# Optimization experiments

Hardware: AMD Instinct MI355X
Metric: run time of the kernel (lower is better)

Reference implementation:

```python
import jax, jax.numpy as jnp
import numpy as np

HID, HEADS, FF, DEPTH = 1152, 16, 4304, 2
HD = HID // HEADS            # 72
ROT = HD // 2                # 36 (rotary_pos_emb width)
S, NSEG = 2048, 4
EPS = 1e-6


def _layernorm(x, w, b):
    m = jnp.mean(x, axis=-1, keepdims=True)
    xc = x - m
    v = jnp.mean(xc * xc, axis=-1, keepdims=True)
    return xc * jax.lax.rsqrt(v + EPS) * w + b


def _rotate_half(x):
    x1, x2 = jnp.split(x, 2, axis=-1)
    return jnp.concatenate([-x2, x1], axis=-1)


def _apply_rotary(t, freqs):
    # t: [S, H, D], freqs: [S, D/2]
    emb = jnp.concatenate([freqs, freqs], axis=-1)          # [S, D]
    cos = jnp.cos(emb)[:, None, :]
    sin = jnp.sin(emb)[:, None, :]
    return t * cos + _rotate_half(t) * sin


def setup_inputs() -> dict:
    key = jax.random.key(0)
    ks = jax.random.split(key, 16)
    sd = 0.02
    # rotary freqs as in VisionRotaryEmbedding(dim=HD//2): h-pos and w-pos halves
    inv_freq = 1.0 / (10000.0 ** (jnp.arange(0, ROT, 2, dtype=jnp.float32) / ROT))  # [18]
    pos = jnp.arange(S, dtype=jnp.float32)
    hpos, wpos = pos // 32.0, pos % 32.0
    rotary = jnp.concatenate([jnp.outer(hpos, inv_freq), jnp.outer(wpos, inv_freq)], axis=-1)  # [S, 36]
    return {
        "x": jax.random.normal(ks[0], (S, HID), jnp.float32),
        "cu_seqlens": jnp.arange(NSEG + 1, dtype=jnp.int32) * (S // NSEG),
        "rotary_pos_emb": rotary,
        "norm1_w": jnp.ones((DEPTH, HID), jnp.float32),
        "norm1_b": jnp.zeros((DEPTH, HID), jnp.float32),
        "qkv_w": jax.random.normal(ks[1], (DEPTH, 3 * HID, HID), jnp.float32) * sd,
        "qkv_b": jnp.zeros((DEPTH, 3 * HID), jnp.float32),
        "proj_w": jax.random.normal(ks[2], (DEPTH, HID, HID), jnp.float32) * sd,
        "proj_b": jnp.zeros((DEPTH, HID), jnp.float32),
        "norm2_w": jnp.ones((DEPTH, HID), jnp.float32),
        "norm2_b": jnp.zeros((DEPTH, HID), jnp.float32),
        "fc1_w": jax.random.normal(ks[3], (DEPTH, FF, HID), jnp.float32) * sd,
        "fc1_b": jnp.zeros((DEPTH, FF), jnp.float32),
        "fc2_w": jax.random.normal(ks[4], (DEPTH, HID, FF), jnp.float32) * sd,
        "fc2_b": jnp.zeros((DEPTH, HID), jnp.float32),
    }


def _forward(x, cu_seqlens, rotary_pos_emb, norm1_w, norm1_b, qkv_w, qkv_b,
             proj_w, proj_b, norm2_w, norm2_b, fc1_w, fc1_b, fc2_w, fc2_b):
    seq_len = x.shape[0]
    # block-diagonal additive mask from cu_seqlens (same mask the torch loop builds)
    seg = jnp.searchsorted(cu_seqlens, jnp.arange(seq_len, dtype=cu_seqlens.dtype), side="right") - 1
    same = seg[:, None] == seg[None, :]
    bias = jnp.where(same, jnp.float32(0.0), jnp.finfo(jnp.float32).min)  # [S, S]
    scale = 1.0 / np.sqrt(HD)
    for d in range(DEPTH):
        # --- attention ---
        h = _layernorm(x, norm1_w[d], norm1_b[d])
        qkv = (h @ qkv_w[d].T + qkv_b[d]).reshape(seq_len, 3, HEADS, HD)
        q, k, v = qkv[:, 0], qkv[:, 1], qkv[:, 2]           # [S, H, D]
        q = _apply_rotary(q, rotary_pos_emb)
        k = _apply_rotary(k, rotary_pos_emb)
        scores = jnp.einsum("qhd,khd->hqk", q, k) * scale + bias[None]
        probs = jax.nn.softmax(scores.astype(jnp.float32), axis=-1).astype(q.dtype)
        attn = jnp.einsum("hqk,khd->qhd", probs, v).reshape(seq_len, HID)
        x = x + attn @ proj_w[d].T + proj_b[d]
        # --- MLP (gelu tanh approx) ---
        h2 = _layernorm(x, norm2_w[d], norm2_b[d])
        x = x + jax.nn.gelu(h2 @ fc1_w[d].T + fc1_b[d], approximate=True) @ fc2_w[d].T + fc2_b[d]
    return x


def reference(x, cu_seqlens, rotary_pos_emb, norm1_w, norm1_b, qkv_w, qkv_b,
              proj_w, proj_b, norm2_w, norm2_b, fc1_w, fc1_b, fc2_w, fc2_b):
    return _forward(x, cu_seqlens, rotary_pos_emb, norm1_w, norm1_b, qkv_w, qkv_b,
                    proj_w, proj_b, norm2_w, norm2_b, fc1_w, fc1_b, fc2_w, fc2_b)
```

## Files before the change

kernel.cpp:

```cpp
#include <hip/hip_runtime.h>

#define S_LEN 2048
#define HID   1152
#define HEADS 16
#define HD    72
#define ROT   36
#define LD3   3456
#define FF    4304
#define FFP   4320

typedef short s16x8 __attribute__((ext_vector_type(8)));
typedef short s16x4 __attribute__((ext_vector_type(4)));
typedef float f32x4 __attribute__((ext_vector_type(4)));
typedef short bf_t;

__device__ __forceinline__ short f2b(float f) {
  unsigned u = __float_as_uint(f);
  u += 0x7fffu + ((u >> 16) & 1u);
  return (short)(u >> 16);
}
__device__ __forceinline__ float b2f(short h) {
  return __uint_as_float(((unsigned)(unsigned short)h) << 16);
}
__device__ __forceinline__ float gelu_f(float x) {
  float t = tanhf(0.7978845608028654f * (x + 0.044715f * x * x * x));
  return 0.5f * x * (1.0f + t);
}

typedef const __attribute__((address_space(1))) void* gas_p;
typedef __attribute__((address_space(3))) void* las_p;
__device__ __forceinline__ void gload16(const void* g, void* l) {
  __builtin_amdgcn_global_load_lds((gas_p)g, (las_p)l, 16, 0, 0);
}

__global__ __launch_bounds__(256) void convw4_kernel(
    const float* __restrict__ src, int N, int K,
    bf_t* __restrict__ dst, int Kpad)
{
  int idx = blockIdx.x * 256 + threadIdx.x;
  int kq = Kpad >> 2;
  if (idx >= N * kq) return;
  int n = idx / kq, k = (idx % kq) << 2;
  s16x4 o;
  if (k + 3 < K) {
    float4 v = *(const float4*)(src + (size_t)n * K + k);
    o[0] = f2b(v.x); o[1] = f2b(v.y); o[2] = f2b(v.z); o[3] = f2b(v.w);
  } else {
#pragma unroll
    for (int j = 0; j < 4; j++) {
      int kk = k + j;
      o[j] = (kk < K) ? f2b(src[(size_t)n * K + kk]) : (short)0;
    }
  }
  *(s16x4*)(dst + (size_t)n * Kpad + k) = o;
}

__global__ __launch_bounds__(256) void costab_kernel(
    const float* __restrict__ rot, float* __restrict__ ct, float* __restrict__ st)
{
  int i = blockIdx.x * 256 + threadIdx.x;
  if (i < S_LEN * ROT) { float f = rot[i]; ct[i] = cosf(f); st[i] = sinf(f); }
}

__global__ __launch_bounds__(256) void ln_kernel(
    const float* __restrict__ x, const float* __restrict__ wgt,
    const float* __restrict__ bia, bf_t* __restrict__ outb)
{
  const int row = blockIdx.x, tid = threadIdx.x;
  const float4* xr = (const float4*)(x + (size_t)row * HID);
  float4 a = xr[tid];
  float4 b2 = make_float4(0.f, 0.f, 0.f, 0.f);
  const bool has2 = tid < 32;
  if (has2) b2 = xr[256 + tid];
  float s = a.x + a.y + a.z + a.w + b2.x + b2.y + b2.z + b2.w;
  float q = a.x*a.x + a.y*a.y + a.z*a.z + a.w*a.w
          + b2.x*b2.x + b2.y*b2.y + b2.z*b2.z + b2.w*b2.w;
  for (int mk = 32; mk; mk >>= 1) { s += __shfl_xor(s, mk); q += __shfl_xor(q, mk); }
  __shared__ float red[16];
  if ((tid & 63) == 0) { red[tid >> 6] = s; red[8 + (tid >> 6)] = q; }
  __syncthreads();
  if (tid == 0) {
    red[4]  = red[0] + red[1] + red[2] + red[3];
    red[12] = red[8] + red[9] + red[10] + red[11];
  }
  __syncthreads();
  float mean = red[4] * (1.0f / HID);
  float var  = red[12] * (1.0f / HID) - mean * mean;
  float rstd = rsqrtf(var + 1e-6f);
  const float4* w4 = (const float4*)wgt;
  const float4* b4 = (const float4*)bia;
  s16x4* o4 = (s16x4*)(outb + (size_t)row * HID);
  {
    float4 wv = w4[tid], bv = b4[tid];
    s16x4 o;
    o[0] = f2b((a.x - mean) * rstd * wv.x + bv.x);
    o[1] = f2b((a.y - mean) * rstd * wv.y + bv.y);
    o[2] = f2b((a.z - mean) * rstd * wv.z + bv.z);
    o[3] = f2b((a.w - mean) * rstd * wv.w + bv.w);
    o4[tid] = o;
  }
  if (has2) {
    float4 wv = w4[256 + tid], bv = b4[256 + tid];
    s16x4 o;
    o[0] = f2b((b2.x - mean) * rstd * wv.x + bv.x);
    o[1] = f2b((b2.y - mean) * rstd * wv.y + bv.y);
    o[2] = f2b((b2.z - mean) * rstd * wv.z + bv.z);
    o[3] = f2b((b2.w - mean) * rstd * wv.w + bv.w);
    o4[256 + tid] = o;
  }
}

__global__ __launch_bounds__(256) void rotary_kernel(
    bf_t* __restrict__ qkv, const float* __restrict__ ct, const float* __restrict__ st)
{
  int idx = blockIdx.x * 256 + threadIdx.x;
  if (idx >= S_LEN * HEADS * ROT) return;
  int t = idx / (HEADS * ROT);
  int r = idx % (HEADS * ROT);
  int h = r / ROT, dd = r % ROT;
  float c = ct[t * ROT + dd], s = st[t * ROT + dd];
  size_t base = (size_t)t * LD3 + h * HD + dd;
  float q1 = b2f(qkv[base]),        q2 = b2f(qkv[base + ROT]);
  float k1 = b2f(qkv[base + HID]),  k2 = b2f(qkv[base + HID + ROT]);
  const float scale = 0.11785113019775793f;
  qkv[base]             = f2b((q1 * c - q2 * s) * scale);
  qkv[base + ROT]       = f2b((q2 * c + q1 * s) * scale);
  qkv[base + HID]       = f2b(k1 * c - k2 * s);
  qkv[base + HID + ROT] = f2b(k2 * c + k1 * s);
}

template<int MODE>
__global__ __launch_bounds__(256, 4) void gemm1(
    const bf_t* __restrict__ A, int lda,
    const bf_t* __restrict__ B, int ldb,
    const float* __restrict__ bias, int nbias,
    void* outp, int ldc, int nvalid, int K, int kchunk)
{
  __shared__ __align__(16) bf_t As[128 * 32];
  __shared__ __align__(16) bf_t Bs[128 * 32];
  const int tid = threadIdx.x;
  const int l = tid & 63, w = tid >> 6;
  const int lr = l & 15, lg = l >> 4;
  const int wm = (w >> 1) * 64, wn = (w & 1) * 64;

  unsigned gx = gridDim.x, gy = gridDim.y, gz = gridDim.z;
  unsigned nwg = gx * gy * gz;
  unsigned lin = (blockIdx.z * gy + blockIdx.y) * gx + blockIdx.x;
  if ((nwg & 7u) == 0u) {
    unsigned q = nwg >> 3;
    lin = (lin & 7u) * q + (lin >> 3);
  }
  const unsigned bz = lin / (gx * gy);
  const unsigned rem = lin % (gx * gy);
  const unsigned by = rem / gx, bx = rem % gx;

  const int rowA0 = by * 128, colB0 = bx * 128;
  const int kb0 = bz * kchunk;
  int kb1 = kb0 + kchunk; if (kb1 > K) kb1 = K;

  const int o1 = tid * 16, o2 = o1 + 4096;
  const int r1 = o1 >> 6, c1 = o1 & 63;
  const int r2 = o2 >> 6, c2 = o2 & 63;
  const char* Ab = (const char*)A;
  const char* Bb = (const char*)B;

  f32x4 acc[4][4] = {};

  for (int kb = kb0; kb < kb1; kb += 32) {
    gload16(Ab + ((size_t)(rowA0 + r1) * lda + kb) * 2 + c1, (char*)As + o1);
    gload16(Ab + ((size_t)(rowA0 + r2) * lda + kb) * 2 + c2, (char*)As + o2);
    gload16(Bb + ((size_t)(colB0 + r1) * ldb + kb) * 2 + c1, (char*)Bs + o1);
    gload16(Bb + ((size_t)(colB0 + r2) * ldb + kb) * 2 + c2, (char*)Bs + o2);
    asm volatile("s_waitcnt vmcnt(0)" ::: "memory");
    __syncthreads();
    s16x8 af[4], bv[4];
#pragma unroll
    for (int mt = 0; mt < 4; mt++) af[mt] = *(const s16x8*)&As[(wm + mt * 16 + lr) * 32 + lg * 8];
#pragma unroll
    for (int nt = 0; nt < 4; nt++) bv[nt] = *(const s16x8*)&Bs[(wn + nt * 16 + lr) * 32 + lg * 8];
#pragma unroll
    for (int mt = 0; mt < 4; mt++)
#pragma unroll
      for (int nt = 0; nt < 4; nt++)
        acc[mt][nt] = __builtin_amdgcn_mfma_f32_16x16x32_bf16(af[mt], bv[nt], acc[mt][nt], 0, 0, 0);
    __syncthreads();
  }

#pragma unroll
  for (int mt = 0; mt < 4; mt++) {
    const int rr = rowA0 + wm + mt * 16 + lg * 4;
#pragma unroll
    for (int nt = 0; nt < 4; nt++) {
      const int cc = colB0 + wn + nt * 16 + lr;
      const float bvl = (MODE == 3) ? 0.0f : ((cc < nbias) ? bias[cc] : 0.0f);
#pragma unroll
      for (int i = 0; i < 4; i++) {
        float v = acc[mt][nt][i] + bvl;
        const int row = rr + i;
        if (MODE == 0) {
          ((bf_t*)outp)[(size_t)row * ldc + cc] = f2b(v);
        } else if (MODE == 2) {
          if (cc < nvalid)      ((bf_t*)outp)[(size_t)row * ldc + cc] = f2b(gelu_f(v));
          else if (cc < ldc)    ((bf_t*)outp)[(size_t)row * ldc + cc] = 0;
        } else {
          float* P = (float*)outp + (size_t)bz * ((size_t)S_LEN * ldc);
          P[(size_t)row * ldc + cc] = v;
        }
      }
    }
  }
}

template<int MODE>
__global__ __launch_bounds__(256, 4) void gemm2(
    const bf_t* __restrict__ A, int lda,
    const bf_t* __restrict__ B, int ldb,
    const float* __restrict__ bias, int nbias,
    void* outp, int ldc, int nvalid, int K, int kchunk)
{
  __shared__ __align__(16) bf_t As[2][128 * 32];
  __shared__ __align__(16) bf_t Bs[2][64 * 32];
  const int tid = threadIdx.x;
  const int l = tid & 63, w = tid >> 6;
  const int lr = l & 15, lg = l >> 4;
  const int wm = (w >> 1) * 64, wn = (w & 1) * 32;

  unsigned gx = gridDim.x, gy = gridDim.y, gz = gridDim.z;
  unsigned nwg = gx * gy * gz;
  unsigned lin = (blockIdx.z * gy + blockIdx.y) * gx + blockIdx.x;
  if ((nwg & 7u) == 0u) {
    unsigned q = nwg >> 3;
    lin = (lin & 7u) * q + (lin >> 3);
  }
  const unsigned bz = lin / (gx * gy);
  const unsigned rem = lin % (gx * gy);
  const unsigned by = rem / gx, bx = rem % gx;

  const int rowA0 = by * 128, colB0 = bx * 64;
  const int kb0 = bz * kchunk;
  int kb1 = kb0 + kchunk; if (kb1 > K) kb1 = K;

  const int oA1 = tid * 16, oA2 = oA1 + 4096;
  const int rA1 = oA1 >> 6, cA1 = oA1 & 63;
  const int rA2 = rA1 + 64;
  const int oB = tid * 16;
  const int rB = oB >> 6, cB = oB & 63;
  const char* Ab = (const char*)A;
  const char* Bb = (const char*)B;

#define STAGE(buf, kk) do { \
    gload16(Ab + ((size_t)(rowA0 + rA1) * lda + (kk)) * 2 + cA1, (char*)As[buf] + oA1); \
    gload16(Ab + ((size_t)(rowA0 + rA2) * lda + (kk)) * 2 + cA1, (char*)As[buf] + oA2); \
    gload16(Bb + ((size_t)(colB0 + rB)  * ldb + (kk)) * 2 + cB,  (char*)Bs[buf] + oB);  \
  } while (0)

  f32x4 acc[4][2] = {};

  STAGE(0, kb0);
  asm volatile("s_waitcnt vmcnt(0)" ::: "memory");
  __builtin_amdgcn_s_barrier();
  __builtin_amdgcn_sched_barrier(0);

  int cur = 0;
  for (int kb = kb0; kb < kb1; kb += 32) {
    if (kb + 32 < kb1) STAGE(cur ^ 1, kb + 32);
    s16x8 af[4], bv[2];
#pragma unroll
    for (int mt = 0; mt < 4; mt++)
      af[mt] = *(const s16x8*)&As[cur][(wm + mt * 16 + lr) * 32 + lg * 8];
#pragma unroll
    for (int nt = 0; nt < 2; nt++)
      bv[nt] = *(const s16x8*)&Bs[cur][(wn + nt * 16 + lr) * 32 + lg * 8];
    asm volatile("s_waitcnt lgkmcnt(0)" ::: "memory");
    __builtin_amdgcn_sched_barrier(0);
#pragma unroll
    for (int mt = 0; mt < 4; mt++)
#pragma unroll
      for (int nt = 0; nt < 2; nt++)
        acc[mt][nt] = __builtin_amdgcn_mfma_f32_16x16x32_bf16(af[mt], bv[nt], acc[mt][nt], 0, 0, 0);
    asm volatile("s_waitcnt vmcnt(0)" ::: "memory");
    __builtin_amdgcn_s_barrier();
    __builtin_amdgcn_sched_barrier(0);
    cur ^= 1;
  }
#undef STAGE

#pragma unroll
  for (int mt = 0; mt < 4; mt++) {
    const int rr = rowA0 + wm + mt * 16 + lg * 4;
#pragma unroll
    for (int nt = 0; nt < 2; nt++) {
      const int cc = colB0 + wn + nt * 16 + lr;
      const float bvl = (cc < nbias) ? bias[cc] : 0.0f;
#pragma unroll
      for (int i = 0; i < 4; i++) {
        float v = acc[mt][nt][i] + bvl;
        const int row = rr + i;
        if (MODE == 0) {
          ((bf_t*)outp)[(size_t)row * ldc + cc] = f2b(v);
        } else if (MODE == 2) {
          if (cc < nvalid)      ((bf_t*)outp)[(size_t)row * ldc + cc] = f2b(gelu_f(v));
          else if (cc < ldc)    ((bf_t*)outp)[(size_t)row * ldc + cc] = 0;
        } else {
          float* P = (float*)outp + (size_t)bz * ((size_t)S_LEN * ldc);
          P[(size_t)row * ldc + cc] = v;
        }
      }
    }
  }
}

__global__ __launch_bounds__(256) void reduce_kernel(
    const float* __restrict__ part, const float* __restrict__ bias,
    const float* __restrict__ resid, float* __restrict__ outp)
{
  int idx = blockIdx.x * 256 + threadIdx.x;
  if (idx >= S_LEN * HID / 4) return;
  float4 r = ((const float4*)resid)[idx];
  float4 bv = ((const float4*)bias)[idx % (HID / 4)];
  float sx = r.x + bv.x, sy = r.y + bv.y, sz = r.z + bv.z, sw = r.w + bv.w;
#pragma unroll
  for (int p = 0; p < 4; p++) {
    float4 v = ((const float4*)(part + (size_t)p * S_LEN * HID))[idx];
    sx += v.x; sy += v.y; sz += v.z; sw += v.w;
  }
  ((float4*)outp)[idx] = make_float4(sx, sy, sz, sw);
}

#define QSTR 104
#define VSTR 76
#define PSTR 72
__global__ __launch_bounds__(256, 2) void attn_kernel(
    const bf_t* __restrict__ qkv, const int* __restrict__ cu, int nseg,
    bf_t* __restrict__ outb)
{
  __shared__ __align__(16) bf_t Qs[64 * QSTR];
  __shared__ __align__(16) bf_t Ks[2][64 * QSTR];
  __shared__ __align__(16) bf_t VTs[2][80 * VSTR];
  __shared__ __align__(16) bf_t Pb[4][16 * PSTR];
  const int tid = threadIdx.x;
  const int l = tid & 63, w = tid >> 6;
  const int lr = l & 15, lg = l >> 4;
  const int h = blockIdx.y;
  const int qbase = blockIdx.x * 64;

  int kstart = 0, kend = S_LEN;
  for (int s2 = 0; s2 < nseg; s2++) {
    int a = cu[s2], b = cu[s2 + 1];
    if (qbase >= a && qbase < b) { kstart = a; kend = b; }
  }

  for (int i = tid; i < 64 * QSTR; i += 256)
    if ((i % QSTR) >= HD) { Qs[i] = 0; Ks[0][i] = 0; Ks[1][i] = 0; }
  for (int i = tid; i < 80 * VSTR; i += 256)
    if ((i / VSTR) >= HD) { VTs[0][i] = 0; VTs[1][i] = 0; }
  for (int c = tid; c < 576; c += 256) {
    int r = c / 9, j = c % 9;
    *(s16x8*)&Qs[r * QSTR + j * 8] =
        *(const s16x8*)&qkv[(size_t)(qbase + r) * LD3 + h * HD + j * 8];
  }
  {
#pragma unroll
    for (int u = 0; u < 3; u++) {
      int c = tid + u * 256;
      if (c < 576) {
        int r = c / 9, j = c % 9;
        int gr = kstart + r; if (gr >= kend) gr = kend - 1;
        *(s16x8*)&Ks[0][r * QSTR + j * 8] =
            *(const s16x8*)&qkv[(size_t)gr * LD3 + HID + h * HD + j * 8];
      }
    }
#pragma unroll
    for (int u = 0; u < 3; u++) {
      int c = tid + u * 256;
      if (c < 576) {
        int r = c & 63, j = c >> 6;
        int gr = kstart + r; if (gr >= kend) gr = kend - 1;
        s16x8 v = *(const s16x8*)&qkv[(size_t)gr * LD3 + 2 * HID + h * HD + j * 8];
#pragma unroll
        for (int jj = 0; jj < 8; jj++) VTs[0][(j * 8 + jj) * VSTR + r] = v[jj];
      }
    }
  }
  __syncthreads();

  s16x8 qf[3];
#pragma unroll
  for (int ks = 0; ks < 3; ks++)
    qf[ks] = *(const s16x8*)&Qs[(w * 16 + lr) * QSTR + ks * 32 + lg * 8];

  float m_i[4], l_i[4];
  f32x4 Of[5] = {};
#pragma unroll
  for (int i = 0; i < 4; i++) { m_i[i] = -1e30f; l_i[i] = 0.0f; }

  const int ntile = (kend - kstart + 63) >> 6;
  int cur = 0;
  for (int t = 0; t < ntile; t++) {
    const int kb = kstart + t * 64;
    const bool more = (t + 1 < ntile);

    s16x8 kreg[3], vreg[3];
    if (more) {
      const int nb = kb + 64;
#pragma unroll
      for (int u = 0; u < 3; u++) {
        int c = tid + u * 256;
        if (c < 576) {
          int r = c / 9, j = c % 9;
          int gr = nb + r; if (gr >= kend) gr = kend - 1;
          kreg[u] = *(const s16x8*)&qkv[(size_t)gr * LD3 + HID + h * HD + j * 8];
        }
      }
#pragma unroll
      for (int u = 0; u < 3; u++) {
        int c = tid + u * 256;
        if (c < 576) {
          int r = c & 63, j = c >> 6;
          int gr = nb + r; if (gr >= kend) gr = kend - 1;
          vreg[u] = *(const s16x8*)&qkv[(size_t)gr * LD3 + 2 * HID + h * HD + j * 8];
        }
      }
    }

    f32x4 sc[4] = {};
#pragma unroll
    for (int kc = 0; kc < 4; kc++) {
#pragma unroll
      for (int ks = 0; ks < 3; ks++) {
        s16x8 kf = *(const s16x8*)&Ks[cur][(kc * 16 + lr) * QSTR + ks * 32 + lg * 8];
        sc[kc] = __builtin_amdgcn_mfma_f32_16x16x32_bf16(qf[ks], kf, sc[kc], 0, 0, 0);
      }
    }
#pragma unroll
    for (int kc = 0; kc < 4; kc++) {
      if ((kb + kc * 16 + lr) >= kend) {
#pragma unroll
        for (int i = 0; i < 4; i++) sc[kc][i] = -1e30f;
      }
    }
    float tmax[4], scl[4], rs[4];
#pragma unroll
    for (int i = 0; i < 4; i++) {
      float tm = fmaxf(fmaxf(sc[0][i], sc[1][i]), fmaxf(sc[2][i], sc[3][i]));
#pragma unroll
      for (int d2 = 1; d2 < 16; d2 <<= 1) tm = fmaxf(tm, __shfl_xor(tm, d2));
      tmax[i] = tm;
    }
#pragma unroll
    for (int i = 0; i < 4; i++) {
      float mn = fmaxf(m_i[i], tmax[i]);
      scl[i] = __expf(m_i[i] - mn);
      m_i[i] = mn;
      rs[i] = 0.0f;
    }
#pragma unroll
    for (int kc = 0; kc < 4; kc++)
#pragma unroll
      for (int i = 0; i < 4; i++) {
        float p = __expf(sc[kc][i] - m_i[i]);
        sc[kc][i] = p;
        rs[i] += p;
      }
#pragma unroll
    for (int i = 0; i < 4; i++) {
#pragma unroll
      for (int d2 = 1; d2 < 16; d2 <<= 1) rs[i] += __shfl_xor(rs[i], d2);
      l_i[i] = l_i[i] * scl[i] + rs[i];
    }
#pragma unroll
    for (int nt = 0; nt < 5; nt++)
#pragma unroll
      for (int i = 0; i < 4; i++) Of[nt][i] *= scl[i];
#pragma unroll
    for (int kc = 0; kc < 4; kc++)
#pragma unroll
      for (int i = 0; i < 4; i++)
        Pb[w][(lg * 4 + i) * PSTR + kc * 16 + lr] = f2b(sc[kc][i]);
    asm volatile("s_waitcnt lgkmcnt(0)" ::: "memory");
    __builtin_amdgcn_sched_barrier(0);
    s16x8 pf[2];
#pragma unroll
    for (int k2 = 0; k2 < 2; k2++)
      pf[k2] = *(const s16x8*)&Pb[w][lr * PSTR + k2 * 32 + lg * 8];
#pragma unroll
    for (int nt = 0; nt < 5; nt++) {
#pragma unroll
      for (int k2 = 0; k2 < 2; k2++) {
        const int vb = (nt * 16 + lr) * VSTR + k2 * 32 + lg * 8;
        s16x4 va = *(const s16x4*)&VTs[cur][vb];
        s16x4 vb2 = *(const s16x4*)&VTs[cur][vb + 4];
        s16x8 vf;
        vf[0] = va[0]; vf[1] = va[1]; vf[2] = va[2]; vf[3] = va[3];
        vf[4] = vb2[0]; vf[5] = vb2[1]; vf[6] = vb2[2]; vf[7] = vb2[3];
        Of[nt] = __builtin_amdgcn_mfma_f32_16x16x32_bf16(pf[k2], vf, Of[nt], 0, 0, 0);
      }
    }

    if (more) {
#pragma unroll
      for (int u = 0; u < 3; u++) {
        int c = tid + u * 256;
        if (c < 576) {
          int r = c / 9, j = c % 9;
          *(s16x8*)&Ks[cur ^ 1][r * QSTR + j * 8] = kreg[u];
        }
      }
#pragma unroll
      for (int u = 0; u < 3; u++) {
        int c = tid + u * 256;
        if (c < 576) {
          int r = c & 63, j = c >> 6;
#pragma unroll
          for (int jj = 0; jj < 8; jj++)
            VTs[cur ^ 1][(j * 8 + jj) * VSTR + r] = vreg[u][jj];
        }
      }
    }
    __syncthreads();
    cur ^= 1;
  }

  float inv[4];
#pragma unroll
  for (int i = 0; i < 4; i++) inv[i] = 1.0f / l_i[i];
#pragma unroll
  for (int nt = 0; nt < 5; nt++) {
    int cc = nt * 16 + lr;
    if (cc < HD) {
#pragma unroll
      for (int i = 0; i < 4; i++) {
        int row = qbase + w * 16 + lg * 4 + i;
        outb[(size_t)row * HID + h * HD + cc] = f2b(Of[nt][i] * inv[i]);
      }
    }
  }
}

extern "C" void kernel_launch(void* const* d_in, const int* in_sizes, int n_in,
                              void* d_out, int out_size, void* d_ws, size_t ws_size,
                              hipStream_t stream) {
  const float* x     = (const float*)d_in[0];
  const int*   cu    = (const int*)d_in[1];
  const float* rotab = (const float*)d_in[2];
  const float* n1w   = (const float*)d_in[3];
  const float* n1b   = (const float*)d_in[4];
  const float* qkvw  = (const float*)d_in[5];
  const float* qkvb  = (const float*)d_in[6];
  const float* projw = (const float*)d_in[7];
  const float* projb = (const float*)d_in[8];
  const float* n2w   = (const float*)d_in[9];
  const float* n2b   = (const float*)d_in[10];
  const float* fc1w  = (const float*)d_in[11];
  const float* fc1b  = (const float*)d_in[12];
  const float* fc2w  = (const float*)d_in[13];
  const float* fc2b  = (const float*)d_in[14];
  float* out = (float*)d_out;
  char* ws = (char*)d_ws;

  size_t off = 0;
  float* xbuf = (float*)(ws + off); off += (size_t)S_LEN * HID * 4;
  bf_t* hbf   = (bf_t*)(ws + off);  off += (size_t)S_LEN * HID * 2;
  bf_t* qkvbf = (bf_t*)(ws + off);
  bf_t* ff1bf = (bf_t*)(ws + off);  off += (size_t)S_LEN * FFP * 2;
  bf_t* attnbf= (bf_t*)(ws + off);  off += (size_t)S_LEN * HID * 2;
  bf_t* wslot = (bf_t*)(ws + off);  off += (size_t)4352 * 1152 * 2;
  float* ctab = (float*)(ws + off); off += (size_t)S_LEN * ROT * 4;
  float* stab = (float*)(ws + off); off += (size_t)S_LEN * ROT * 4;
  float* part = (float*)(ws + off); off += (size_t)4 * S_LEN * HID * 4;

  costab_kernel<<<(S_LEN * ROT + 255) / 256, 256, 0, stream>>>(rotab, ctab, stab);

  const int nseg = in_sizes[1] - 1;
  const int RED_GRID = (S_LEN * HID / 4 + 255) / 256;

  for (int d = 0; d < 2; d++) {
    const float* xin = (d == 0) ? x : xbuf;
    ln_kernel<<<S_LEN, 256, 0, stream>>>(xin, n1w + d * HID, n1b + d * HID, hbf);
    convw4_kernel<<<(LD3 * HID / 4 + 255) / 256, 256, 0, stream>>>(
        qkvw + (size_t)d * LD3 * HID, LD3, HID, wslot, HID);
    gemm2<0><<<dim3(LD3 / 64, 16), 256, 0, stream>>>(
        hbf, HID, wslot, HID, qkvb + (size_t)d * LD3, LD3, qkvbf, LD3, LD3, HID, HID);
    rotary_kernel<<<(S_LEN * HEADS * ROT + 255) / 256, 256, 0, stream>>>(qkvbf, ctab, stab);
    attn_kernel<<<dim3(S_LEN / 64, HEADS), 256, 0, stream>>>(qkvbf, cu, nseg, attnbf);
    convw4_kernel<<<(HID * HID / 4 + 255) / 256, 256, 0, stream>>>(
        projw + (size_t)d * HID * HID, HID, HID, wslot, HID);
    gemm1<3><<<dim3(HID / 128, 16, 4), 256, 0, stream>>>(
        attnbf, HID, wslot, HID, nullptr, 0, part, HID, HID, HID, 288);
    reduce_kernel<<<RED_GRID, 256, 0, stream>>>(part, projb + (size_t)d * HID, xin, xbuf);
    ln_kernel<<<S_LEN, 256, 0, stream>>>(xbuf, n2w + d * HID, n2b + d * HID, hbf);
    convw4_kernel<<<(FF * HID / 4 + 255) / 256, 256, 0, stream>>>(
        fc1w + (size_t)d * FF * HID, FF, HID, wslot, HID);
    gemm2<2><<<dim3((FFP + 63) / 64, 16), 256, 0, stream>>>(
        hbf, HID, wslot, HID, fc1b + (size_t)d * FF, FF, ff1bf, FFP, FF, HID, HID);
    convw4_kernel<<<(HID * FFP / 4 + 255) / 256, 256, 0, stream>>>(
        fc2w + (size_t)d * HID * FF, HID, FF, wslot, FFP);
    float* outp = (d == 1) ? out : xbuf;
    gemm1<3><<<dim3(HID / 128, 16, 4), 256, 0, stream>>>(
        ff1bf, FFP, wslot, FFP, nullptr, 0, part, HID, HID, FFP, 1088);
    reduce_kernel<<<RED_GRID, 256, 0, stream>>>(part, fc2b + (size_t)d * HID, xbuf, outp);
  }
}
```

Measured before the change: 436.0 us.

## Fuse split-K reduction with layernorm and batch weight conversions per layer

```diff
diff --git a/kernel.cpp b/kernel.cpp
--- a/kernel.cpp
+++ b/kernel.cpp
@@ -33,26 +33,43 @@
   __builtin_amdgcn_global_load_lds((gas_p)g, (las_p)l, 16, 0, 0);
 }
 
-__global__ __launch_bounds__(256) void convw4_kernel(
-    const float* __restrict__ src, int N, int K,
-    bf_t* __restrict__ dst, int Kpad)
+#define QKV_OFF 0
+#define P_OFF   (3456 * 1152)
+#define F1_OFF  (P_OFF + 1152 * 1152)
+#define F2_OFF  (F1_OFF + 4352 * 1152)
+#define ARENA_ELEMS (F2_OFF + 1152 * 4320)
+#define GA_Q  (8960 * 288)
+#define TOT_Q (GA_Q + 1152 * 1080)
+
+__global__ __launch_bounds__(256) void convw_all(
+    const float* __restrict__ qkvw, const float* __restrict__ projw,
+    const float* __restrict__ fc1w, const float* __restrict__ fc2w,
+    bf_t* __restrict__ arena)
 {
   int idx = blockIdx.x * 256 + threadIdx.x;
-  int kq = Kpad >> 2;
-  if (idx >= N * kq) return;
-  int n = idx / kq, k = (idx % kq) << 2;
-  s16x4 o;
-  if (k + 3 < K) {
-    float4 v = *(const float4*)(src + (size_t)n * K + k);
-    o[0] = f2b(v.x); o[1] = f2b(v.y); o[2] = f2b(v.z); o[3] = f2b(v.w);
+  if (idx >= TOT_Q) return;
+  if (idx < GA_Q) {
+    int row = idx / 288, kq = (idx % 288) * 4;
+    const float* s = nullptr; bf_t* d;
+    if (row < 3456)      { s = qkvw + (size_t)row * 1152;  d = arena + (size_t)row * 1152; }
+    else if (row < 4608) { int r = row - 3456; s = projw + (size_t)r * 1152; d = arena + P_OFF + (size_t)r * 1152; }
+    else                 { int r = row - 4608; d = arena + F1_OFF + (size_t)r * 1152;
+                           if (r < FF) s = fc1w + (size_t)r * 1152; }
+    s16x4 o;
+    if (s) { float4 v = *(const float4*)(s + kq);
+             o[0] = f2b(v.x); o[1] = f2b(v.y); o[2] = f2b(v.z); o[3] = f2b(v.w); }
+    else   { o[0] = 0; o[1] = 0; o[2] = 0; o[3] = 0; }
+    *(s16x4*)(d + kq) = o;
   } else {
-#pragma unroll
-    for (int j = 0; j < 4; j++) {
-      int kk = k + j;
-      o[j] = (kk < K) ? f2b(src[(size_t)n * K + kk]) : (short)0;
-    }
-  }
-  *(s16x4*)(dst + (size_t)n * Kpad + k) = o;
+    int q = idx - GA_Q;
+    int r = q / 1080, kq = (q % 1080) * 4;
+    s16x4 o;
+    if (kq < FF) {
+      float4 v = *(const float4*)(fc2w + (size_t)r * FF + kq);
+      o[0] = f2b(v.x); o[1] = f2b(v.y); o[2] = f2b(v.z); o[3] = f2b(v.w);
+    } else { o[0] = 0; o[1] = 0; o[2] = 0; o[3] = 0; }
+    *(s16x4*)(arena + F2_OFF + (size_t)r * FFP + kq) = o;
+  }
 }
 
 __global__ __launch_bounds__(256) void costab_kernel(
@@ -110,6 +127,82 @@
   }
 }
 
+__global__ __launch_bounds__(256) void redln_kernel(
+    const float* __restrict__ part, const float* __restrict__ bias,
+    const float* __restrict__ resid, float* __restrict__ xout,
+    bf_t* __restrict__ hout, const float* __restrict__ lnw,
+    const float* __restrict__ lnb, int do_ln)
+{
+  const int row = blockIdx.x, tid = threadIdx.x;
+  const size_t base = (size_t)row * 288;
+  const float4* r4 = (const float4*)resid;
+  const float4* b4 = (const float4*)bias;
+  const float4* p4 = (const float4*)part;
+  const bool has2 = tid < 32;
+
+  float4 a, c;
+  {
+    float4 r = r4[base + tid], bv = b4[tid];
+    a = make_float4(r.x + bv.x, r.y + bv.y, r.z + bv.z, r.w + bv.w);
+#pragma unroll
+    for (int p = 0; p < 4; p++) {
+      float4 v = p4[(size_t)p * S_LEN * 288 + base + tid];
+      a.x += v.x; a.y += v.y; a.z += v.z; a.w += v.w;
+    }
+  }
+  c = make_float4(0.f, 0.f, 0.f, 0.f);
+  if (has2) {
+    float4 r = r4[base + 256 + tid], bv = b4[256 + tid];
+    c = make_float4(r.x + bv.x, r.y + bv.y, r.z + bv.z, r.w + bv.w);
+#pragma unroll
+    for (int p = 0; p < 4; p++) {
+      float4 v = p4[(size_t)p * S_LEN * 288 + base + 256 + tid];
+      c.x += v.x; c.y += v.y; c.z += v.z; c.w += v.w;
+    }
+  }
+  ((float4*)xout)[base + tid] = a;
+  if (has2) ((float4*)xout)[base + 256 + tid] = c;
+
+  if (!do_ln) return;
+
+  float s = a.x + a.y + a.z + a.w + c.x + c.y + c.z + c.w;
+  float q = a.x*a.x + a.y*a.y + a.z*a.z + a.w*a.w
+          + c.x*c.x + c.y*c.y + c.z*c.z + c.w*c.w;
+  for (int mk = 32; mk; mk >>= 1) { s += __shfl_xor(s, mk); q += __shfl_xor(q, mk); }
+  __shared__ float red[16];
+  if ((tid & 63) == 0) { red[tid >> 6] = s; red[8 + (tid >> 6)] = q; }
+  __syncthreads();
+  if (tid == 0) {
+    red[4]  = red[0] + red[1] + red[2] + red[3];
+    red[12] = red[8] + red[9] + red[10] + red[11];
+  }
+  __syncthreads();
+  float mean = red[4] * (1.0f / HID);
+  float var  = red[12] * (1.0f / HID) - mean * mean;
+  float rstd = rsqrtf(var + 1e-6f);
+  const float4* w4 = (const float4*)lnw;
+  const float4* lb4 = (const float4*)lnb;
+  s16x4* o4 = (s16x4*)(hout + (size_t)row * HID);
+  {
+    float4 wv = w4[tid], bv = lb4[tid];
+    s16x4 o;
+    o[0] = f2b((a.x - mean) * rstd * wv.x + bv.x);
+    o[1] = f2b((a.y - mean) * rstd * wv.y + bv.y);
+    o[2] = f2b((a.z - mean) * rstd * wv.z + bv.z);
+    o[3] = f2b((a.w - mean) * rstd * wv.w + bv.w);
+    o4[tid] = o;
+  }
+  if (has2) {
+    float4 wv = w4[256 + tid], bv = lb4[256 + tid];
+    s16x4 o;
+    o[0] = f2b((c.x - mean) * rstd * wv.x + bv.x);
+    o[1] = f2b((c.y - mean) * rstd * wv.y + bv.y);
+    o[2] = f2b((c.z - mean) * rstd * wv.z + bv.z);
+    o[3] = f2b((c.w - mean) * rstd * wv.w + bv.w);
+    o4[256 + tid] = o;
+  }
+}
+
 __global__ __launch_bounds__(256) void rotary_kernel(
     bf_t* __restrict__ qkv, const float* __restrict__ ct, const float* __restrict__ st)
 {
@@ -308,23 +401,6 @@
       }
     }
   }
-}
-
-__global__ __launch_bounds__(256) void reduce_kernel(
-    const float* __restrict__ part, const float* __restrict__ bias,
-    const float* __restrict__ resid, float* __restrict__ outp)
-{
-  int idx = blockIdx.x * 256 + threadIdx.x;
-  if (idx >= S_LEN * HID / 4) return;
-  float4 r = ((const float4*)resid)[idx];
-  float4 bv = ((const float4*)bias)[idx % (HID / 4)];
-  float sx = r.x + bv.x, sy = r.y + bv.y, sz = r.z + bv.z, sw = r.w + bv.w;
-#pragma unroll
-  for (int p = 0; p < 4; p++) {
-    float4 v = ((const float4*)(part + (size_t)p * S_LEN * HID))[idx];
-    sx += v.x; sy += v.y; sz += v.z; sw += v.w;
-  }
-  ((float4*)outp)[idx] = make_float4(sx, sy, sz, sw);
 }
 
 #define QSTR 104
@@ -564,7 +640,7 @@
   bf_t* qkvbf = (bf_t*)(ws + off);
   bf_t* ff1bf = (bf_t*)(ws + off);  off += (size_t)S_LEN * FFP * 2;
   bf_t* attnbf= (bf_t*)(ws + off);  off += (size_t)S_LEN * HID * 2;
-  bf_t* wslot = (bf_t*)(ws + off);  off += (size_t)4352 * 1152 * 2;
+  bf_t* arena = (bf_t*)(ws + off);  off += (size_t)ARENA_ELEMS * 2;
   float* ctab = (float*)(ws + off); off += (size_t)S_LEN * ROT * 4;
   float* stab = (float*)(ws + off); off += (size_t)S_LEN * ROT * 4;
   float* part = (float*)(ws + off); off += (size_t)4 * S_LEN * HID * 4;
@@ -572,32 +648,35 @@
   costab_kernel<<<(S_LEN * ROT + 255) / 256, 256, 0, stream>>>(rotab, ctab, stab);
 
   const int nseg = in_sizes[1] - 1;
-  const int RED_GRID = (S_LEN * HID / 4 + 255) / 256;
 
   for (int d = 0; d < 2; d++) {
     const float* xin = (d == 0) ? x : xbuf;
-    ln_kernel<<<S_LEN, 256, 0, stream>>>(xin, n1w + d * HID, n1b + d * HID, hbf);
-    convw4_kernel<<<(LD3 * HID / 4 + 255) / 256, 256, 0, stream>>>(
-        qkvw + (size_t)d * LD3 * HID, LD3, HID, wslot, HID);
+    convw_all<<<(TOT_Q + 255) / 256, 256, 0, stream>>>(
+        qkvw + (size_t)d * LD3 * HID, projw + (size_t)d * HID * HID,
+        fc1w + (size_t)d * FF * HID, fc2w + (size_t)d * HID * FF, arena);
+    if (d == 0)
+      ln_kernel<<<S_LEN, 256, 0, stream>>>(x, n1w, n1b, hbf);
     gemm2<0><<<dim3(LD3 / 64, 16), 256, 0, stream>>>(
-        hbf, HID, wslot, HID, qkvb + (size_t)d * LD3, LD3, qkvbf, LD3, LD3, HID, HID);
+        hbf, HID, arena + QKV_OFF, HID, qkvb + (size_t)d * LD3, LD3,
+        qkvbf, LD3, LD3, HID, HID);
     rotary_kernel<<<(S_LEN * HEADS * ROT + 255) / 256, 256, 0, stream>>>(qkvbf, ctab, stab);
     attn_kernel<<<dim3(S_LEN / 64, HEADS), 256, 0, stream>>>(qkvbf, cu, nseg, attnbf);
-    convw4_kernel<<<(HID * HID / 4 + 255) / 256, 256, 0, stream>>>(
-        projw + (size_t)d * HID * HID, HID, HID, wslot, HID);
     gemm1<3><<<dim3(HID / 128, 16, 4), 256, 0, stream>>>(
-        attnbf, HID, wslot, HID, nullptr, 0, part, HID, HID, HID, 288);
-    reduce_kernel<<<RED_GRID, 256, 0, stream>>>(part, projb + (size_t)d * HID, xin, xbuf);
-    ln_kernel<<<S_LEN, 256, 0, stream>>>(xbuf, n2w + d * HID, n2b + d * HID, hbf);
-    convw4_kernel<<<(FF * HID / 4 + 255) / 256, 256, 0, stream>>>(
-        fc1w + (size_t)d * FF * HID, FF, HID, wslot, HID);
+        attnbf, HID, arena + P_OFF, HID, nullptr, 0, part, HID, HID, HID, 288);
+    redln_kernel<<<S_LEN, 256, 0, stream>>>(
+        part, projb + (size_t)d * HID, xin, xbuf, hbf,
+        n2w + (size_t)d * HID, n2b + (size_t)d * HID, 1);
     gemm2<2><<<dim3((FFP + 63) / 64, 16), 256, 0, stream>>>(
-        hbf, HID, wslot, HID, fc1b + (size_t)d * FF, FF, ff1bf, FFP, FF, HID, HID);
-    convw4_kernel<<<(HID * FFP / 4 + 255) / 256, 256, 0, stream>>>(
-        fc2w + (size_t)d * HID * FF, HID, FF, wslot, FFP);
-    float* outp = (d == 1) ? out : xbuf;
+        hbf, HID, arena + F1_OFF, HID, fc1b + (size_t)d * FF, FF,
+        ff1bf, FFP, FF, HID, HID);
     gemm1<3><<<dim3(HID / 128, 16, 4), 256, 0, stream>>>(
-        ff1bf, FFP, wslot, FFP, nullptr, 0, part, HID, HID, FFP, 1088);
-    reduce_kernel<<<RED_GRID, 256, 0, stream>>>(part, fc2b + (size_t)d * HID, xbuf, outp);
-  }
-}
+        ff1bf, FFP, arena + F2_OFF, FFP, nullptr, 0, part, HID, HID, FFP, 1088);
+    if (d == 0) {
+      redln_kernel<<<S_LEN, 256, 0, stream>>>(
+          part, fc2b, xbuf, xbuf, hbf, n1w + HID, n1b + HID, 1);
+    } else {
+      redln_kernel<<<S_LEN, 256, 0, stream>>>(
+          part, fc2b + (size_t)HID, xbuf, out, nullptr, nullptr, nullptr, 0);
+    }
+  }
+}
```

Result: faster. 410.8 us (-5.8%).
